# Kernel optimization log

Hardware: AMD Instinct MI355X
Metric: run time of the kernel (lower is better)

Reference implementation:

```python
import jax, jax.numpy as jnp
import numpy as np

N_NODES = 100000
N_EDGES = 3200000
NFEAT, HID, NCLASS = 256, 32, 16


def setup_inputs() -> dict:
    key = jax.random.key(0)
    ks = jax.random.split(key, 6)
    x = jax.random.normal(ks[0], (N_NODES, NFEAT), dtype=jnp.float32)
    edge_index = jax.random.randint(ks[1], (2, N_EDGES), 0, N_NODES, dtype=jnp.int64)
    edge_weight = jax.random.uniform(ks[2], (N_EDGES,), dtype=jnp.float32)
    # Glorot-ish init for the two GCNConv linear weights; bias zeros (PyG default init zeros bias)
    W1 = jax.random.normal(ks[3], (NFEAT, HID), dtype=jnp.float32) * (1.0 / np.sqrt(NFEAT))
    b1 = jnp.zeros((HID,), dtype=jnp.float32)
    W2 = jax.random.normal(ks[4], (HID, NCLASS), dtype=jnp.float32) * (1.0 / np.sqrt(HID))
    b2 = jnp.zeros((NCLASS,), dtype=jnp.float32)
    return {"x": x, "edge_index": edge_index, "edge_weight": edge_weight,
            "W1": W1, "b1": b1, "W2": W2, "b2": b2}


def _gcn_norm(row, col, w, n):
    """PyG gcn_norm: add self-loops (weight 1), symmetric normalization."""
    loop = jnp.arange(n, dtype=row.dtype)
    row = jnp.concatenate([row, loop])
    col = jnp.concatenate([col, loop])
    w = jnp.concatenate([w, jnp.ones((n,), dtype=w.dtype)])
    deg = jax.ops.segment_sum(w, col, num_segments=n)  # degree at target nodes
    dinv = jnp.where(deg > 0, jax.lax.rsqrt(deg), 0.0)
    norm = dinv[row] * w * dinv[col]
    return row, col, norm


def _gcn_conv(x, W, b, row, col, norm, n):
    xw = x @ W                                  # [N, out]
    msg = xw[row] * norm[:, None]               # gather at source + scale
    out = jax.ops.segment_sum(msg, col, num_segments=n)  # scatter-add at target
    return out + b


def reference(x, edge_index, edge_weight, W1, b1, W2, b2):
    n = x.shape[0]
    row, col, norm = _gcn_norm(edge_index[0], edge_index[1], edge_weight, n)
    h = jax.nn.relu(_gcn_conv(x, W1, b1, row, col, norm, n))
    # dropout is identity in eval mode
    logits = _gcn_conv(h, W2, b2, row, col, norm, n)
    return jax.nn.log_softmax(logits, axis=1)
```

## Files before the change

kernel.cpp:

```cpp
#include <hip/hip_runtime.h>

#define N_NODES 100000
#define N_EDGES 3200000
#define NFEAT 256
#define HID 32
#define NCLASS 16

#define NB 64
#define CHUNK (N_EDGES / NB)
#define RN2 32768
#define NR2 ((N_NODES + RN2 - 1) / RN2)

#define SCAN_TPB 256
#define SCAN_EPB 1024
#define SCAN_NBLK ((N_NODES + SCAN_EPB - 1) / SCAN_EPB)

#define XPAD 133

__device__ inline unsigned short f2bf(float f) {
    unsigned u = __float_as_uint(f);
    u += 0x7FFFu + ((u >> 16) & 1u);
    return (unsigned short)(u >> 16);
}
__device__ inline float bf2f(unsigned short s) {
    return __uint_as_float((unsigned)s << 16);
}
__device__ inline void bf8_unpack(uint4 g, float* f) {
    f[0] = __uint_as_float(g.x << 16); f[1] = __uint_as_float(g.x & 0xFFFF0000u);
    f[2] = __uint_as_float(g.y << 16); f[3] = __uint_as_float(g.y & 0xFFFF0000u);
    f[4] = __uint_as_float(g.z << 16); f[5] = __uint_as_float(g.z & 0xFFFF0000u);
    f[6] = __uint_as_float(g.w << 16); f[7] = __uint_as_float(g.w & 0xFFFF0000u);
}

__global__ __launch_bounds__(1024) void k_count(const int* __restrict__ col,
                                                unsigned* __restrict__ H) {
    __shared__ unsigned hist[RN2 / 2];
    int t = threadIdx.x, b = blockIdx.x, r = blockIdx.y;
    int base = r * RN2;
    const int* cc = col + (size_t)b * CHUNK;
    for (int i = t; i < RN2 / 2; i += 1024) hist[i] = 0;
    __syncthreads();
    for (int i = t; i < CHUNK; i += 1024) {
        unsigned d = (unsigned)cc[i] - (unsigned)base;
        if (d < RN2) atomicAdd(&hist[d >> 1], 1u << ((d & 1) * 16));
    }
    __syncthreads();
    int lim = min(RN2, N_NODES - base);
    unsigned* Hb = H + (size_t)b * N_NODES;
    for (int i = t; i < lim; i += 1024)
        Hb[base + i] = (hist[i >> 1] >> ((i & 1) * 16)) & 0xFFFFu;
}

__global__ void k_rowsum(const unsigned* __restrict__ H, int* __restrict__ cnt) {
    int n = blockIdx.x * 256 + threadIdx.x;
    if (n >= N_NODES) return;
    unsigned s = 0;
    #pragma unroll 8
    for (int b = 0; b < NB; ++b) s += H[(size_t)b * N_NODES + n];
    cnt[n] = (int)s;
}

__global__ __launch_bounds__(SCAN_TPB) void k_scanA(const int* __restrict__ cnt,
                                                    int* __restrict__ offs,
                                                    int* __restrict__ bsum) {
    __shared__ int s[SCAN_TPB];
    int t = threadIdx.x;
    int base = blockIdx.x * SCAN_EPB + t * 4;
    int v0 = (base + 0 < N_NODES) ? cnt[base + 0] : 0;
    int v1 = (base + 1 < N_NODES) ? cnt[base + 1] : 0;
    int v2 = (base + 2 < N_NODES) ? cnt[base + 2] : 0;
    int v3 = (base + 3 < N_NODES) ? cnt[base + 3] : 0;
    int sum = v0 + v1 + v2 + v3;
    s[t] = sum;
    __syncthreads();
    for (int off = 1; off < SCAN_TPB; off <<= 1) {
        int x = (t >= off) ? s[t - off] : 0;
        __syncthreads();
        s[t] += x;
        __syncthreads();
    }
    int excl = s[t] - sum;
    if (t == SCAN_TPB - 1) bsum[blockIdx.x] = s[t];
    int run = excl;
    if (base + 0 < N_NODES) offs[base + 0] = run; run += v0;
    if (base + 1 < N_NODES) offs[base + 1] = run; run += v1;
    if (base + 2 < N_NODES) offs[base + 2] = run; run += v2;
    if (base + 3 < N_NODES) offs[base + 3] = run;
}

__global__ __launch_bounds__(128) void k_scanB(int* __restrict__ bsum) {
    __shared__ int s[128];
    int t = threadIdx.x;
    int v = (t < SCAN_NBLK) ? bsum[t] : 0;
    s[t] = v;
    __syncthreads();
    for (int off = 1; off < 128; off <<= 1) {
        int x = (t >= off) ? s[t - off] : 0;
        __syncthreads();
        s[t] += x;
        __syncthreads();
    }
    if (t < SCAN_NBLK) bsum[t] = s[t] - v;
}

__global__ __launch_bounds__(SCAN_TPB) void k_scanC(int* __restrict__ offs,
                                                    const int* __restrict__ bsum) {
    int t = threadIdx.x;
    int add = bsum[blockIdx.x];
    int base = blockIdx.x * SCAN_EPB + t * 4;
    #pragma unroll
    for (int i = 0; i < 4; ++i) {
        int idx = base + i;
        if (idx < N_NODES) offs[idx] += add;
    }
    if (blockIdx.x == 0 && t == 0) offs[N_NODES] = N_EDGES;
}

__global__ void k_bprefix(unsigned* __restrict__ H, const int* __restrict__ offs) {
    int n = blockIdx.x * 256 + threadIdx.x;
    if (n >= N_NODES) return;
    unsigned run = (unsigned)offs[n];
    for (int b = 0; b < NB; ++b) {
        size_t idx = (size_t)b * N_NODES + n;
        unsigned v = H[idx];
        H[idx] = run;
        run += v;
    }
}

__global__ __launch_bounds__(1024) void k_place(const int* __restrict__ col,
                                                const unsigned* __restrict__ B,
                                                unsigned* __restrict__ perm) {
    __shared__ unsigned rk[RN2 / 2];
    int t = threadIdx.x, b = blockIdx.x, r = blockIdx.y;
    int base = r * RN2;
    size_t eb = (size_t)b * CHUNK;
    const unsigned* Bb = B + (size_t)b * N_NODES;
    for (int i = t; i < RN2 / 2; i += 1024) rk[i] = 0;
    __syncthreads();
    for (int i = t; i < CHUNK; i += 1024) {
        int c = col[eb + i];
        unsigned d = (unsigned)c - (unsigned)base;
        if (d < RN2) {
            unsigned old = atomicAdd(&rk[d >> 1], 1u << ((d & 1) * 16));
            unsigned rr = (old >> ((d & 1) * 16)) & 0xFFFFu;
            perm[eb + i] = Bb[c] + rr;
        }
    }
}

__global__ void k_emit(const int* __restrict__ row, const float* __restrict__ w,
                       const unsigned* __restrict__ perm, float2* __restrict__ ein) {
    int e = blockIdx.x * 256 + threadIdx.x;
    if (e < N_EDGES) ein[perm[e]] = make_float2(__int_as_float(row[e]), w[e]);
}

__global__ void k_deg(const float2* __restrict__ ein, const int* __restrict__ offs,
                      float* __restrict__ dinv) {
    int idx = blockIdx.x * 256 + threadIdx.x;
    int n = idx >> 2, l = idx & 3;
    if (n >= N_NODES) return;
    int s = offs[n], e = offs[n + 1];
    float sum = 0.f;
    for (int p = s + l; p < e; p += 4) sum += ein[p].y;
    sum += __shfl_xor(sum, 1, 4);
    sum += __shfl_xor(sum, 2, 4);
    if (l == 0) dinv[n] = rsqrtf(1.0f + sum);
}

__global__ __launch_bounds__(256) void k_gemm1s(const float* __restrict__ x,
                                                const float* __restrict__ W1,
                                                unsigned short* __restrict__ xwp) {
    __shared__ float sWc[32 * HID];
    __shared__ float sX[32 * XPAD];
    int t = threadIdx.x;
    long rowbase = (long)blockIdx.x * 128;
    int kbase = blockIdx.y * 128;
    unsigned short* xw = xwp + (size_t)blockIdx.y * N_NODES * HID;
    int tr = t >> 3;
    int tc = t & 7;
    float acc[4][4] = {};
    for (int k0 = kbase; k0 < kbase + 128; k0 += 32) {
        *(float4*)&sWc[t * 4] = *(const float4*)&W1[k0 * HID + t * 4];
        #pragma unroll
        for (int p = 0; p < 4; ++p) {
            int rt = (t >> 3) + p * 32;
            int kk = (t & 7) * 4;
            long grow = rowbase + rt;
            float4 v = make_float4(0.f, 0.f, 0.f, 0.f);
            if (grow < N_NODES) v = *(const float4*)&x[grow * NFEAT + k0 + kk];
            sX[(kk + 0) * XPAD + rt] = v.x; sX[(kk + 1) * XPAD + rt] = v.y;
            sX[(kk + 2) * XPAD + rt] = v.z; sX[(kk + 3) * XPAD + rt] = v.w;
        }
        __syncthreads();
        #pragma unroll 8
        for (int kk = 0; kk < 32; ++kk) {
            float xv[4], wv[4];
            xv[0] = sX[kk * XPAD + tr * 4 + 0];
            xv[1] = sX[kk * XPAD + tr * 4 + 1];
            xv[2] = sX[kk * XPAD + tr * 4 + 2];
            xv[3] = sX[kk * XPAD + tr * 4 + 3];
            *(float4*)&wv[0] = *(float4*)&sWc[kk * HID + tc * 4];
            #pragma unroll
            for (int m = 0; m < 4; ++m)
                #pragma unroll
                for (int n = 0; n < 4; ++n)
                    acc[m][n] = fmaf(xv[m], wv[n], acc[m][n]);
        }
        __syncthreads();
    }
    #pragma unroll
    for (int m = 0; m < 4; ++m) {
        long r = rowbase + tr * 4 + m;
        if (r < N_NODES) {
            ushort4 o;
            o.x = f2bf(acc[m][0]); o.y = f2bf(acc[m][1]);
            o.z = f2bf(acc[m][2]); o.w = f2bf(acc[m][3]);
            *(ushort4*)&xw[r * HID + tc * 4] = o;
        }
    }
}

__global__ void k_comb(const unsigned short* __restrict__ xwp,
                       ushort4* __restrict__ xwb) {
    int i = blockIdx.x * 256 + threadIdx.x;
    const ushort4* p0 = (const ushort4*)xwp;
    const ushort4* p1 = p0 + 800000;
    ushort4 a = p0[i], b = p1[i];
    ushort4 o;
    o.x = f2bf(bf2f(a.x) + bf2f(b.x));
    o.y = f2bf(bf2f(a.y) + bf2f(b.y));
    o.z = f2bf(bf2f(a.z) + bf2f(b.z));
    o.w = f2bf(bf2f(a.w) + bf2f(b.w));
    xwb[i] = o;
}

__global__ __launch_bounds__(256) void k_gather1(const unsigned short* __restrict__ xwb,
                                                 const float* __restrict__ dinv,
                                                 const float2* __restrict__ ein,
                                                 const int* __restrict__ offs,
                                                 const float* __restrict__ b1,
                                                 float* __restrict__ h) {
    int idx = blockIdx.x * 256 + threadIdx.x;
    int n = idx >> 2, l = idx & 3;
    if (n >= N_NODES) return;
    int c8 = l * 8;
    const uint4* xb = (const uint4*)xwb;
    float di = dinv[n];
    float acc[8], f[8];
    bf8_unpack(xb[(long)n * 4 + l], f);
    #pragma unroll
    for (int k = 0; k < 8; ++k) acc[k] = f[k] * di;
    int s = offs[n], e = offs[n + 1];
    for (int p0 = s; p0 < e; p0 += 8) {
        int pl0 = p0 + l, pl1 = p0 + 4 + l;
        float2 pr0 = (pl0 < e) ? ein[pl0] : make_float2(__int_as_float(n), 0.f);
        float2 pr1 = (pl1 < e) ? ein[pl1] : make_float2(__int_as_float(n), 0.f);
        int r0 = __float_as_int(pr0.x), r1 = __float_as_int(pr1.x);
        pr0.y *= dinv[r0];
        pr1.y *= dinv[r1];
        #pragma unroll
        for (int j = 0; j < 4; ++j) {
            int r = __shfl(r0, j, 4);
            float nm = __shfl(pr0.y, j, 4);
            bf8_unpack(xb[(long)r * 4 + l], f);
            #pragma unroll
            for (int k = 0; k < 8; ++k) acc[k] = fmaf(f[k], nm, acc[k]);
        }
        #pragma unroll
        for (int j = 0; j < 4; ++j) {
            int r = __shfl(r1, j, 4);
            float nm = __shfl(pr1.y, j, 4);
            bf8_unpack(xb[(long)r * 4 + l], f);
            #pragma unroll
            for (int k = 0; k < 8; ++k) acc[k] = fmaf(f[k], nm, acc[k]);
        }
    }
    float4 bb0 = *(const float4*)&b1[c8];
    float4 bb1 = *(const float4*)&b1[c8 + 4];
    float4 o0, o1;
    o0.x = fmaxf(fmaf(acc[0], di, bb0.x), 0.f);
    o0.y = fmaxf(fmaf(acc[1], di, bb0.y), 0.f);
    o0.z = fmaxf(fmaf(acc[2], di, bb0.z), 0.f);
    o0.w = fmaxf(fmaf(acc[3], di, bb0.w), 0.f);
    o1.x = fmaxf(fmaf(acc[4], di, bb1.x), 0.f);
    o1.y = fmaxf(fmaf(acc[5], di, bb1.y), 0.f);
    o1.z = fmaxf(fmaf(acc[6], di, bb1.z), 0.f);
    o1.w = fmaxf(fmaf(acc[7], di, bb1.w), 0.f);
    *(float4*)&h[(long)n * HID + c8] = o0;
    *(float4*)&h[(long)n * HID + c8 + 4] = o1;
}

__global__ __launch_bounds__(256) void k_gemm2(const float* __restrict__ h,
                                               const float* __restrict__ W2,
                                               unsigned short* __restrict__ hwb) {
    __shared__ float sH[64][33];
    __shared__ float sW2[HID * NCLASS];
    int t = threadIdx.x;
    if (t < 128) {
        int idx = t * 4;
        *(float4*)&sW2[idx] = *(const float4*)&W2[idx];
    }
    long base = (long)blockIdx.x * 64;
    #pragma unroll
    for (int i = 0; i < 2; ++i) {
        int idx = t + i * 256;
        int rt = idx >> 3, kk = (idx & 7) * 4;
        long gr = base + rt;
        float4 v = make_float4(0.f, 0.f, 0.f, 0.f);
        if (gr < N_NODES) v = *(const float4*)&h[gr * HID + kk];
        sH[rt][kk + 0] = v.x; sH[rt][kk + 1] = v.y;
        sH[rt][kk + 2] = v.z; sH[rt][kk + 3] = v.w;
    }
    __syncthreads();
    int r = t >> 2, c4 = (t & 3) * 4;
    float acc[4] = {};
    #pragma unroll
    for (int k = 0; k < HID; ++k) {
        float hv = sH[r][k];
        float wv[4];
        *(float4*)&wv[0] = *(float4*)&sW2[k * NCLASS + c4];
        #pragma unroll
        for (int n = 0; n < 4; ++n) acc[n] = fmaf(hv, wv[n], acc[n]);
    }
    long gr = base + r;
    if (gr < N_NODES) {
        ushort4 o;
        o.x = f2bf(acc[0]); o.y = f2bf(acc[1]);
        o.z = f2bf(acc[2]); o.w = f2bf(acc[3]);
        *(ushort4*)&hwb[gr * NCLASS + c4] = o;
    }
}

__global__ __launch_bounds__(256) void k_gather2(const unsigned short* __restrict__ hwb,
                                                 const float* __restrict__ dinv,
                                                 const float2* __restrict__ ein,
                                                 const int* __restrict__ offs,
                                                 const float* __restrict__ b2,
                                                 float* __restrict__ out) {
    int idx = blockIdx.x * 256 + threadIdx.x;
    int n = idx >> 1, l = idx & 1;
    if (n >= N_NODES) return;
    int c8 = l * 8;
    const uint4* hb = (const uint4*)hwb;
    float di = dinv[n];
    float acc[8], f[8];
    bf8_unpack(hb[(long)n * 2 + l], f);
    #pragma unroll
    for (int k = 0; k < 8; ++k) acc[k] = f[k] * di;
    int s = offs[n], e = offs[n + 1];
    for (int p0 = s; p0 < e; p0 += 8) {
        float2 pr[4];
        int rr[4];
        #pragma unroll
        for (int k = 0; k < 4; ++k) {
            int pl = p0 + k * 2 + l;
            pr[k] = (pl < e) ? ein[pl] : make_float2(__int_as_float(n), 0.f);
            rr[k] = __float_as_int(pr[k].x);
            pr[k].y *= dinv[rr[k]];
        }
        #pragma unroll
        for (int k = 0; k < 4; ++k) {
            #pragma unroll
            for (int j = 0; j < 2; ++j) {
                int r = __shfl(rr[k], j, 2);
                float nm = __shfl(pr[k].y, j, 2);
                bf8_unpack(hb[(long)r * 2 + l], f);
                #pragma unroll
                for (int q = 0; q < 8; ++q) acc[q] = fmaf(f[q], nm, acc[q]);
            }
        }
    }
    float4 bb0 = *(const float4*)&b2[c8];
    float4 bb1 = *(const float4*)&b2[c8 + 4];
    float v[8];
    v[0] = fmaf(acc[0], di, bb0.x); v[1] = fmaf(acc[1], di, bb0.y);
    v[2] = fmaf(acc[2], di, bb0.z); v[3] = fmaf(acc[3], di, bb0.w);
    v[4] = fmaf(acc[4], di, bb1.x); v[5] = fmaf(acc[5], di, bb1.y);
    v[6] = fmaf(acc[6], di, bb1.z); v[7] = fmaf(acc[7], di, bb1.w);
    float m = v[0];
    #pragma unroll
    for (int k = 1; k < 8; ++k) m = fmaxf(m, v[k]);
    m = fmaxf(m, __shfl_xor(m, 1, 2));
    float sum = 0.f;
    #pragma unroll
    for (int k = 0; k < 8; ++k) sum += __expf(v[k] - m);
    sum += __shfl_xor(sum, 1, 2);
    float ls = m + __logf(sum);
    float4 o0 = make_float4(v[0] - ls, v[1] - ls, v[2] - ls, v[3] - ls);
    float4 o1 = make_float4(v[4] - ls, v[5] - ls, v[6] - ls, v[7] - ls);
    *(float4*)&out[(long)n * NCLASS + c8] = o0;
    *(float4*)&out[(long)n * NCLASS + c8 + 4] = o1;
}

extern "C" void kernel_launch(void* const* d_in, const int* in_sizes, int n_in,
                              void* d_out, int out_size, void* d_ws, size_t ws_size,
                              hipStream_t stream) {
    const float* x  = (const float*)d_in[0];
    const int*   ei = (const int*)d_in[1];
    const float* w  = (const float*)d_in[2];
    const float* W1 = (const float*)d_in[3];
    const float* b1 = (const float*)d_in[4];
    const float* W2 = (const float*)d_in[5];
    const float* b2 = (const float*)d_in[6];
    float* out = (float*)d_out;

    const int* row = ei;
    const int* col = ei + N_EDGES;

    float* ws = (float*)d_ws;
    float2* ein = (float2*)ws;
    unsigned* H = (unsigned*)(ws + 2 * (size_t)N_EDGES);
    unsigned* perm = (unsigned*)(ws + 2 * (size_t)N_EDGES + (size_t)NB * N_NODES);
    float* h = (float*)perm;
    float* dinv = ws + 2 * (size_t)N_EDGES + (size_t)NB * N_NODES + N_EDGES;
    int* cnt = (int*)(dinv + N_NODES);
    int* offs = cnt + N_NODES;
    int* bsum = offs + N_NODES + 1;
    size_t xwp_off = (size_t)(2 * (size_t)N_EDGES + (size_t)NB * N_NODES + N_EDGES
                              + 3 * N_NODES + 1 + 128);
    xwp_off = (xwp_off + 3) & ~(size_t)3;
    unsigned short* xwp = (unsigned short*)(ws + xwp_off);
    unsigned short* xwb = (unsigned short*)(ws + xwp_off + 3200000);
    unsigned short* hwb = xwb + (size_t)N_NODES * HID;

    const int B = 256;

    k_count<<<dim3(NB, NR2), 1024, 0, stream>>>(col, H);
    k_rowsum<<<(N_NODES + B - 1) / B, B, 0, stream>>>(H, cnt);
    k_scanA<<<SCAN_NBLK, SCAN_TPB, 0, stream>>>(cnt, offs, bsum);
    k_scanB<<<1, 128, 0, stream>>>(bsum);
    k_scanC<<<SCAN_NBLK, SCAN_TPB, 0, stream>>>(offs, bsum);
    k_bprefix<<<(N_NODES + B - 1) / B, B, 0, stream>>>(H, offs);
    k_place<<<dim3(NB, NR2), 1024, 0, stream>>>(col, H, perm);
    k_emit<<<(N_EDGES + B - 1) / B, B, 0, stream>>>(row, w, perm, ein);

    k_deg<<<(N_NODES * 4 + B - 1) / B, B, 0, stream>>>(ein, offs, dinv);

    k_gemm1s<<<dim3((N_NODES + 127) / 128, 2), 256, 0, stream>>>(x, W1, xwp);
    k_comb<<<(N_NODES * HID / 4) / B, B, 0, stream>>>(xwp, (ushort4*)xwb);
    k_gather1<<<(N_NODES * 4 + B - 1) / B, B, 0, stream>>>(xwb, dinv, ein, offs, b1, h);

    k_gemm2<<<(N_NODES + 63) / 64, B, 0, stream>>>(h, W2, hwb);
    k_gather2<<<(N_NODES * 2 + B - 1) / B, B, 0, stream>>>(hwb, dinv, ein, offs, b2, out);
}
```

Baseline: 299.7 us.

## Split layer-1 feature table into halves and gather each half separately

```diff
diff --git a/kernel.cpp b/kernel.cpp
--- a/kernel.cpp
+++ b/kernel.cpp
@@ -222,7 +222,7 @@
 }
 
 __global__ void k_comb(const unsigned short* __restrict__ xwp,
-                       ushort4* __restrict__ xwb) {
+                       ushort4* __restrict__ lo, ushort4* __restrict__ hi) {
     int i = blockIdx.x * 256 + threadIdx.x;
     const ushort4* p0 = (const ushort4*)xwp;
     const ushort4* p1 = p0 + 800000;
@@ -232,52 +232,52 @@
     o.y = f2bf(bf2f(a.y) + bf2f(b.y));
     o.z = f2bf(bf2f(a.z) + bf2f(b.z));
     o.w = f2bf(bf2f(a.w) + bf2f(b.w));
-    xwb[i] = o;
-}
-
-__global__ __launch_bounds__(256) void k_gather1(const unsigned short* __restrict__ xwb,
-                                                 const float* __restrict__ dinv,
-                                                 const float2* __restrict__ ein,
-                                                 const int* __restrict__ offs,
-                                                 const float* __restrict__ b1,
-                                                 float* __restrict__ h) {
+    int n = i >> 3, c = i & 7;
+    if (c < 4) lo[(n << 2) + c] = o;
+    else       hi[(n << 2) + (c - 4)] = o;
+}
+
+__global__ __launch_bounds__(256) void k_gather1h(const unsigned short* __restrict__ tab,
+                                                  const float* __restrict__ dinv,
+                                                  const float2* __restrict__ ein,
+                                                  const int* __restrict__ offs,
+                                                  const float* __restrict__ b1,
+                                                  float* __restrict__ h, int c0) {
     int idx = blockIdx.x * 256 + threadIdx.x;
-    int n = idx >> 2, l = idx & 3;
+    int n = idx >> 1, l = idx & 1;
     if (n >= N_NODES) return;
-    int c8 = l * 8;
-    const uint4* xb = (const uint4*)xwb;
+    const uint4* xb = (const uint4*)tab;
     float di = dinv[n];
     float acc[8], f[8];
-    bf8_unpack(xb[(long)n * 4 + l], f);
+    bf8_unpack(xb[(long)n * 2 + l], f);
     #pragma unroll
     for (int k = 0; k < 8; ++k) acc[k] = f[k] * di;
     int s = offs[n], e = offs[n + 1];
     for (int p0 = s; p0 < e; p0 += 8) {
-        int pl0 = p0 + l, pl1 = p0 + 4 + l;
-        float2 pr0 = (pl0 < e) ? ein[pl0] : make_float2(__int_as_float(n), 0.f);
-        float2 pr1 = (pl1 < e) ? ein[pl1] : make_float2(__int_as_float(n), 0.f);
-        int r0 = __float_as_int(pr0.x), r1 = __float_as_int(pr1.x);
-        pr0.y *= dinv[r0];
-        pr1.y *= dinv[r1];
-        #pragma unroll
-        for (int j = 0; j < 4; ++j) {
-            int r = __shfl(r0, j, 4);
-            float nm = __shfl(pr0.y, j, 4);
-            bf8_unpack(xb[(long)r * 4 + l], f);
+        float2 pr[4];
+        int rr[4];
+        #pragma unroll
+        for (int k = 0; k < 4; ++k) {
+            int pl = p0 + k * 2 + l;
+            pr[k] = (pl < e) ? ein[pl] : make_float2(__int_as_float(n), 0.f);
+            rr[k] = __float_as_int(pr[k].x);
+            pr[k].y *= dinv[rr[k]];
+        }
+        #pragma unroll
+        for (int k = 0; k < 4; ++k) {
             #pragma unroll
-            for (int k = 0; k < 8; ++k) acc[k] = fmaf(f[k], nm, acc[k]);
-        }
-        #pragma unroll
-        for (int j = 0; j < 4; ++j) {
-            int r = __shfl(r1, j, 4);
-            float nm = __shfl(pr1.y, j, 4);
-            bf8_unpack(xb[(long)r * 4 + l], f);
-            #pragma unroll
-            for (int k = 0; k < 8; ++k) acc[k] = fmaf(f[k], nm, acc[k]);
-        }
-    }
-    float4 bb0 = *(const float4*)&b1[c8];
-    float4 bb1 = *(const float4*)&b1[c8 + 4];
+            for (int j = 0; j < 2; ++j) {
+                int r = __shfl(rr[k], j, 2);
+                float nm = __shfl(pr[k].y, j, 2);
+                bf8_unpack(xb[(long)r * 2 + l], f);
+                #pragma unroll
+                for (int q = 0; q < 8; ++q) acc[q] = fmaf(f[q], nm, acc[q]);
+            }
+        }
+    }
+    int fo = c0 + l * 8;
+    float4 bb0 = *(const float4*)&b1[fo];
+    float4 bb1 = *(const float4*)&b1[fo + 4];
     float4 o0, o1;
     o0.x = fmaxf(fmaf(acc[0], di, bb0.x), 0.f);
     o0.y = fmaxf(fmaf(acc[1], di, bb0.y), 0.f);
@@ -287,8 +287,8 @@
     o1.y = fmaxf(fmaf(acc[5], di, bb1.y), 0.f);
     o1.z = fmaxf(fmaf(acc[6], di, bb1.z), 0.f);
     o1.w = fmaxf(fmaf(acc[7], di, bb1.w), 0.f);
-    *(float4*)&h[(long)n * HID + c8] = o0;
-    *(float4*)&h[(long)n * HID + c8 + 4] = o1;
+    *(float4*)&h[(long)n * HID + fo] = o0;
+    *(float4*)&h[(long)n * HID + fo + 4] = o1;
 }
 
 __global__ __launch_bounds__(256) void k_gemm2(const float* __restrict__ h,
@@ -421,8 +421,9 @@
                               + 3 * N_NODES + 1 + 128);
     xwp_off = (xwp_off + 3) & ~(size_t)3;
     unsigned short* xwp = (unsigned short*)(ws + xwp_off);
-    unsigned short* xwb = (unsigned short*)(ws + xwp_off + 3200000);
-    unsigned short* hwb = xwb + (size_t)N_NODES * HID;
+    unsigned short* xwb_lo = (unsigned short*)(ws + xwp_off + 3200000);
+    unsigned short* xwb_hi = xwb_lo + (size_t)N_NODES * 16;
+    unsigned short* hwb = xwb_hi + (size_t)N_NODES * 16;
 
     const int B = 256;
 
@@ -438,8 +439,9 @@
     k_deg<<<(N_NODES * 4 + B - 1) / B, B, 0, stream>>>(ein, offs, dinv);
 
     k_gemm1s<<<dim3((N_NODES + 127) / 128, 2), 256, 0, stream>>>(x, W1, xwp);
-    k_comb<<<(N_NODES * HID / 4) / B, B, 0, stream>>>(xwp, (ushort4*)xwb);
-    k_gather1<<<(N_NODES * 4 + B - 1) / B, B, 0, stream>>>(xwb, dinv, ein, offs, b1, h);
+    k_comb<<<(N_NODES * HID / 4) / B, B, 0, stream>>>(xwp, (ushort4*)xwb_lo, (ushort4*)xwb_hi);
+    k_gather1h<<<(N_NODES * 2 + B - 1) / B, B, 0, stream>>>(xwb_lo, dinv, ein, offs, b1, h, 0);
+    k_gather1h<<<(N_NODES * 2 + B - 1) / B, B, 0, stream>>>(xwb_hi, dinv, ein, offs, b1, h, 16);
 
     k_gemm2<<<(N_NODES + 63) / 64, B, 0, stream>>>(h, W2, hwb);
     k_gather2<<<(N_NODES * 2 + B - 1) / B, B, 0, stream>>>(hwb, dinv, ein, offs, b2, out);
```

Measured after the change: 357.4 us. 19.3% more time.

## Record in-chunk rank during counting, drop place pass, widen gather1 to 8 lanes

Applied to the files above, without the earlier changes.

```diff
diff --git a/kernel.cpp b/kernel.cpp
--- a/kernel.cpp
+++ b/kernel.cpp
@@ -33,16 +33,21 @@
 }
 
 __global__ __launch_bounds__(1024) void k_count(const int* __restrict__ col,
-                                                unsigned* __restrict__ H) {
+                                                unsigned* __restrict__ H,
+                                                unsigned short* __restrict__ pos) {
     __shared__ unsigned hist[RN2 / 2];
     int t = threadIdx.x, b = blockIdx.x, r = blockIdx.y;
     int base = r * RN2;
     const int* cc = col + (size_t)b * CHUNK;
+    unsigned short* pp = pos + (size_t)b * CHUNK;
     for (int i = t; i < RN2 / 2; i += 1024) hist[i] = 0;
     __syncthreads();
     for (int i = t; i < CHUNK; i += 1024) {
         unsigned d = (unsigned)cc[i] - (unsigned)base;
-        if (d < RN2) atomicAdd(&hist[d >> 1], 1u << ((d & 1) * 16));
+        if (d < RN2) {
+            unsigned old = atomicAdd(&hist[d >> 1], 1u << ((d & 1) * 16));
+            pp[i] = (unsigned short)((old >> ((d & 1) * 16)) & 0xFFFFu);
+        }
     }
     __syncthreads();
     int lim = min(RN2, N_NODES - base);
@@ -128,31 +133,16 @@
     }
 }
 
-__global__ __launch_bounds__(1024) void k_place(const int* __restrict__ col,
-                                                const unsigned* __restrict__ B,
-                                                unsigned* __restrict__ perm) {
-    __shared__ unsigned rk[RN2 / 2];
-    int t = threadIdx.x, b = blockIdx.x, r = blockIdx.y;
-    int base = r * RN2;
-    size_t eb = (size_t)b * CHUNK;
-    const unsigned* Bb = B + (size_t)b * N_NODES;
-    for (int i = t; i < RN2 / 2; i += 1024) rk[i] = 0;
-    __syncthreads();
-    for (int i = t; i < CHUNK; i += 1024) {
-        int c = col[eb + i];
-        unsigned d = (unsigned)c - (unsigned)base;
-        if (d < RN2) {
-            unsigned old = atomicAdd(&rk[d >> 1], 1u << ((d & 1) * 16));
-            unsigned rr = (old >> ((d & 1) * 16)) & 0xFFFFu;
-            perm[eb + i] = Bb[c] + rr;
-        }
-    }
-}
-
-__global__ void k_emit(const int* __restrict__ row, const float* __restrict__ w,
-                       const unsigned* __restrict__ perm, float2* __restrict__ ein) {
+__global__ void k_emit(const int* __restrict__ row, const int* __restrict__ col,
+                       const float* __restrict__ w, const unsigned* __restrict__ B,
+                       const unsigned short* __restrict__ pos,
+                       float2* __restrict__ ein) {
     int e = blockIdx.x * 256 + threadIdx.x;
-    if (e < N_EDGES) ein[perm[e]] = make_float2(__int_as_float(row[e]), w[e]);
+    if (e >= N_EDGES) return;
+    int b = e / CHUNK;
+    int c = col[e];
+    unsigned p = B[(size_t)b * N_NODES + c] + (unsigned)pos[e];
+    ein[p] = make_float2(__int_as_float(row[e]), w[e]);
 }
 
 __global__ void k_deg(const float2* __restrict__ ein, const int* __restrict__ offs,
@@ -242,53 +232,36 @@
                                                  const float* __restrict__ b1,
                                                  float* __restrict__ h) {
     int idx = blockIdx.x * 256 + threadIdx.x;
-    int n = idx >> 2, l = idx & 3;
-    if (n >= N_NODES) return;
-    int c8 = l * 8;
-    const uint4* xb = (const uint4*)xwb;
+    int n = idx >> 3, l = idx & 7;
+    int c4 = l * 4;
+    const ushort4* xb = (const ushort4*)xwb;
     float di = dinv[n];
-    float acc[8], f[8];
-    bf8_unpack(xb[(long)n * 4 + l], f);
-    #pragma unroll
-    for (int k = 0; k < 8; ++k) acc[k] = f[k] * di;
+    ushort4 q = xb[(long)n * 8 + l];
+    float4 acc = make_float4(bf2f(q.x) * di, bf2f(q.y) * di,
+                             bf2f(q.z) * di, bf2f(q.w) * di);
     int s = offs[n], e = offs[n + 1];
     for (int p0 = s; p0 < e; p0 += 8) {
-        int pl0 = p0 + l, pl1 = p0 + 4 + l;
-        float2 pr0 = (pl0 < e) ? ein[pl0] : make_float2(__int_as_float(n), 0.f);
-        float2 pr1 = (pl1 < e) ? ein[pl1] : make_float2(__int_as_float(n), 0.f);
-        int r0 = __float_as_int(pr0.x), r1 = __float_as_int(pr1.x);
-        pr0.y *= dinv[r0];
-        pr1.y *= dinv[r1];
+        int pl = p0 + l;
+        float2 pr = (pl < e) ? ein[pl] : make_float2(__int_as_float(n), 0.f);
+        int ri = __float_as_int(pr.x);
+        pr.y *= dinv[ri];
         #pragma unroll
-        for (int j = 0; j < 4; ++j) {
-            int r = __shfl(r0, j, 4);
-            float nm = __shfl(pr0.y, j, 4);
-            bf8_unpack(xb[(long)r * 4 + l], f);
-            #pragma unroll
-            for (int k = 0; k < 8; ++k) acc[k] = fmaf(f[k], nm, acc[k]);
-        }
-        #pragma unroll
-        for (int j = 0; j < 4; ++j) {
-            int r = __shfl(r1, j, 4);
-            float nm = __shfl(pr1.y, j, 4);
-            bf8_unpack(xb[(long)r * 4 + l], f);
-            #pragma unroll
-            for (int k = 0; k < 8; ++k) acc[k] = fmaf(f[k], nm, acc[k]);
-        }
-    }
-    float4 bb0 = *(const float4*)&b1[c8];
-    float4 bb1 = *(const float4*)&b1[c8 + 4];
-    float4 o0, o1;
-    o0.x = fmaxf(fmaf(acc[0], di, bb0.x), 0.f);
-    o0.y = fmaxf(fmaf(acc[1], di, bb0.y), 0.f);
-    o0.z = fmaxf(fmaf(acc[2], di, bb0.z), 0.f);
-    o0.w = fmaxf(fmaf(acc[3], di, bb0.w), 0.f);
-    o1.x = fmaxf(fmaf(acc[4], di, bb1.x), 0.f);
-    o1.y = fmaxf(fmaf(acc[5], di, bb1.y), 0.f);
-    o1.z = fmaxf(fmaf(acc[6], di, bb1.z), 0.f);
-    o1.w = fmaxf(fmaf(acc[7], di, bb1.w), 0.f);
-    *(float4*)&h[(long)n * HID + c8] = o0;
-    *(float4*)&h[(long)n * HID + c8 + 4] = o1;
+        for (int j = 0; j < 8; ++j) {
+            int r = __shfl(ri, j, 8);
+            float nm = __shfl(pr.y, j, 8);
+            ushort4 g = xb[(long)r * 8 + l];
+            acc.x = fmaf(bf2f(g.x), nm, acc.x);
+            acc.y = fmaf(bf2f(g.y), nm, acc.y);
+            acc.z = fmaf(bf2f(g.z), nm, acc.z);
+            acc.w = fmaf(bf2f(g.w), nm, acc.w);
+        }
+    }
+    float4 bb = *(const float4*)&b1[c4];
+    acc.x = fmaxf(fmaf(acc.x, di, bb.x), 0.f);
+    acc.y = fmaxf(fmaf(acc.y, di, bb.y), 0.f);
+    acc.z = fmaxf(fmaf(acc.z, di, bb.z), 0.f);
+    acc.w = fmaxf(fmaf(acc.w, di, bb.w), 0.f);
+    *(float4*)&h[(long)n * HID + c4] = acc;
 }
 
 __global__ __launch_bounds__(256) void k_gemm2(const float* __restrict__ h,
@@ -411,8 +384,8 @@
     float* ws = (float*)d_ws;
     float2* ein = (float2*)ws;
     unsigned* H = (unsigned*)(ws + 2 * (size_t)N_EDGES);
-    unsigned* perm = (unsigned*)(ws + 2 * (size_t)N_EDGES + (size_t)NB * N_NODES);
-    float* h = (float*)perm;
+    unsigned short* pos = (unsigned short*)(ws + 2 * (size_t)N_EDGES + (size_t)NB * N_NODES);
+    float* h = (float*)pos;
     float* dinv = ws + 2 * (size_t)N_EDGES + (size_t)NB * N_NODES + N_EDGES;
     int* cnt = (int*)(dinv + N_NODES);
     int* offs = cnt + N_NODES;
@@ -426,20 +399,19 @@
 
     const int B = 256;
 
-    k_count<<<dim3(NB, NR2), 1024, 0, stream>>>(col, H);
+    k_count<<<dim3(NB, NR2), 1024, 0, stream>>>(col, H, pos);
     k_rowsum<<<(N_NODES + B - 1) / B, B, 0, stream>>>(H, cnt);
     k_scanA<<<SCAN_NBLK, SCAN_TPB, 0, stream>>>(cnt, offs, bsum);
     k_scanB<<<1, 128, 0, stream>>>(bsum);
     k_scanC<<<SCAN_NBLK, SCAN_TPB, 0, stream>>>(offs, bsum);
     k_bprefix<<<(N_NODES + B - 1) / B, B, 0, stream>>>(H, offs);
-    k_place<<<dim3(NB, NR2), 1024, 0, stream>>>(col, H, perm);
-    k_emit<<<(N_EDGES + B - 1) / B, B, 0, stream>>>(row, w, perm, ein);
+    k_emit<<<(N_EDGES + B - 1) / B, B, 0, stream>>>(row, col, w, H, pos, ein);
 
     k_deg<<<(N_NODES * 4 + B - 1) / B, B, 0, stream>>>(ein, offs, dinv);
 
     k_gemm1s<<<dim3((N_NODES + 127) / 128, 2), 256, 0, stream>>>(x, W1, xwp);
     k_comb<<<(N_NODES * HID / 4) / B, B, 0, stream>>>(xwp, (ushort4*)xwb);
-    k_gather1<<<(N_NODES * 4 + B - 1) / B, B, 0, stream>>>(xwb, dinv, ein, offs, b1, h);
+    k_gather1<<<(N_NODES * 8) / B, B, 0, stream>>>(xwb, dinv, ein, offs, b1, h);
 
     k_gemm2<<<(N_NODES + 63) / 64, B, 0, stream>>>(h, W2, hwb);
     k_gather2<<<(N_NODES * 2 + B - 1) / B, B, 0, stream>>>(hwb, dinv, ein, offs, b2, out);
```

Result: faster. 284.4 us (-5.1%).
